# Kernel optimization log

Hardware: AMD Instinct MI355X
Metric: run time of the kernel (lower is better)

Reference implementation:

```python
import jax, jax.numpy as jnp
import numpy as np

B = 4096
N = 8192
LEVEL_SIZES = [8, 128, 2048, 6008]  # sums to N; 4-level taxonomy
EPS = 1e-07


def _build_hierarchy():
    """parent[c] = parent node index (-1 for roots); level_of[c] = depth."""
    rng = np.random.default_rng(0)
    parent = np.full(N, -1, np.int32)
    level_of = np.zeros(N, np.int32)
    off, prev_start, prev_size = 0, 0, 0
    for l, sz in enumerate(LEVEL_SIZES):
        level_of[off:off + sz] = l
        if l > 0:
            parent[off:off + sz] = rng.integers(prev_start, prev_start + prev_size, sz)
        prev_start, prev_size = off, sz
        off += sz
    return parent, level_of


def setup_inputs() -> dict:
    key = jax.random.key(0)
    k1, k2 = jax.random.split(key)
    pred = jax.random.normal(k1, (B, N), dtype=jnp.float32)  # logits
    target = (jax.random.uniform(k2, (B, N)) < 0.02).astype(jnp.float32)
    parent_np, level_np = _build_hierarchy()
    return {
        "pred": pred,
        "target": target,
        "parent": jnp.asarray(parent_np),
        "level_of": jnp.asarray(level_np),
        "mode": 0,  # 0 = EVAL (propagate conditional probs), 1 = TRAIN
    }


def reference(pred, target, parent, level_of, mode):
    p = jax.nn.sigmoid(pred)                      # [B, N]
    parent_clip = jnp.maximum(parent, 0)          # safe gather index for roots
    is_root = parent < 0                          # recursive_relation[-1]

    if mode != 1:  # not 'TRAIN': top-down conditional probability propagation
        pc = p
        for l in range(1, len(LEVEL_SIZES)):
            # pred_clone[:, children(n)] = pred[:, children] * pred_clone[:, n]
            pc = jnp.where(level_of == l, p * pc[:, parent_clip], pc)
        pred_clone = pc
    else:
        pred_clone = None

    # mask[b, c] = 1 if c is a root, or if target[b, parent[c]] == 1
    mask = jnp.where(is_root, jnp.float32(1.0), target[:, parent_clip])

    pcl = jnp.clip(p, EPS, 1.0 - EPS)
    loss = -(jnp.log(pcl) * target + (1.0 - target) * mask * jnp.log(1.0 - pcl))
    loss = loss.sum(axis=1).mean()
    return (loss, pred_clone)
```

## Files before the change

kernel.cpp:

```cpp
#include <hip/hip_runtime.h>


typedef float f4 __attribute__((ext_vector_type(4)));
typedef float f2 __attribute__((ext_vector_type(2)));
typedef int   i4 __attribute__((ext_vector_type(4)));

#define N_NODES 8192
#define L1S 8
#define L2S 136
#define L3S 2184
#define N4   2048
#define L3S4 546
#define WPB 4

__device__ __forceinline__ float frcp(float x) { return __builtin_amdgcn_rcpf(x); }

__device__ __forceinline__ void wave_sync() {
    __builtin_amdgcn_sched_barrier(0);
    asm volatile("s_waitcnt lgkmcnt(0)" ::: "memory");
    __builtin_amdgcn_wave_barrier();
    __builtin_amdgcn_sched_barrier(0);
}

__global__ __launch_bounds__(256, 4) void cs_main(
    const float* __restrict__ pred,
    const float* __restrict__ target,
    const int* __restrict__ parent,
    float* __restrict__ out,
    float* __restrict__ bsum,
    float inv_b, int nrows)
{
    __shared__ float pk_all[WPB * L3S];

    const int tid = threadIdx.x;
    const int lane = tid & 63;
    const int wid = tid >> 6;
    const int b = blockIdx.x * WPB + wid;
    if (b >= nrows) return;

    float* __restrict__ mypk = pk_all + wid * L3S;
    const float* __restrict__ prow = pred + (size_t)b * N_NODES;
    const float* __restrict__ trow = target + (size_t)b * N_NODES;
    float* __restrict__ orow = out + 1 + (size_t)b * N_NODES;
    const f4* __restrict__ Pp = (const f4*)prow;
    const f4* __restrict__ Tp = (const f4*)trow;
    const i4* __restrict__ Qp = (const i4*)parent;

    float lsum = 0.0f;

    {
        int g = lane;
        f4 x4 = Pp[g], t4 = Tp[g];
#pragma unroll
        for (int k = 0; k < 9; ++k) {
            const int gn = g + 64;
            f4 nx, nt;
            const bool hn = (gn < L3S4);
            if (hn) { nx = Pp[gn]; nt = Tp[gn]; }
            if (g < L3S4) {
                f4 pkv;
#pragma unroll
                for (int j = 0; j < 4; ++j) {
                    const float p = frcp(1.0f + __expf(-x4[j]));
                    pkv[j] = t4[j] > 0.5f ? -p : p;
                }
                *(f4*)(mypk + 4 * g) = pkv;
            }
            x4 = nx; t4 = nt; g = gn;
        }
    }

    int gc = L3S4 + lane;
    f4 xA = Pp[gc], tA = Tp[gc]; i4 qA = Qp[gc];
    const int g1 = gc + 64;
    f4 xB = Pp[g1], tB = Tp[g1]; i4 qB = Qp[g1];

    wave_sync();

    if (lane < L1S) {
        const float v = mypk[lane];
        const float p = fabsf(v);
        lsum += (v < 0.0f) ? -__logf(p) : -__logf(1.0f - p);
        orow[lane] = p;
    }

#pragma unroll
    for (int k = 0; k < 2; ++k) {
        const int c = L1S + lane + 64 * k;
        const int pa = parent[c];
        const float v = mypk[c];
        const float pv = mypk[pa];
        const float p = fabsf(v);
        const float cum = p * fabsf(pv);
        const float mask = (pv < 0.0f) ? 1.0f : 0.0f;
        lsum += (v < 0.0f) ? -__logf(p) : mask * (-__logf(1.0f - p));
        orow[c] = cum;
        mypk[c] = (v < 0.0f) ? -cum : cum;
    }
    wave_sync();

#pragma unroll 4
    for (int k = 0; k < 32; ++k) {
        const int c = L2S + lane + 64 * k;
        const int pa = parent[c];
        const float v = mypk[c];
        const float pv = mypk[pa];
        const float p = fabsf(v);
        const float cum = p * fabsf(pv);
        const float mask = (pv < 0.0f) ? 1.0f : 0.0f;
        lsum += (v < 0.0f) ? -__logf(p) : mask * (-__logf(1.0f - p));
        orow[c] = cum;
        mypk[c] = (v < 0.0f) ? -cum : cum;
    }
    wave_sync();

#pragma unroll 4
    for (int k = 0; k < 24; ++k) {
        const int gn = gc + 128 > N4 - 1 ? N4 - 1 : gc + 128;
        f4 nx = Pp[gn], nt = Tp[gn]; i4 nq = Qp[gn];
        if (gc < N4) {
            float rr[4];
#pragma unroll
            for (int j = 0; j < 4; ++j) {
                const float x = xA[j], t = tA[j];
                const float pv = mypk[qA[j]];
                const float mask = (pv < 0.0f) ? 1.0f : 0.0f;
                const float e = __expf(-x);
                const float s = __logf(1.0f + e);
                const float p = frcp(1.0f + e);
                lsum += t * s + (1.0f - t) * mask * (s + x);
                rr[j] = p * fabsf(pv);
            }
            float* slot = orow + 4 * gc;
            slot[0] = rr[0];
            *(f2*)(slot + 1) = f2{rr[1], rr[2]};
            slot[3] = rr[3];
        }
        xA = xB; tA = tB; qA = qB;
        xB = nx; tB = nt; qB = nq;
        gc += 64;
    }

#pragma unroll
    for (int off = 32; off > 0; off >>= 1) lsum += __shfl_down(lsum, off);
    if (lane == 0) {
        if (bsum) bsum[b] = lsum;
        else atomicAdd(out, lsum * inv_b);
    }
}

__global__ __launch_bounds__(256) void cs_finish(
    const float* __restrict__ bsum, float* __restrict__ out,
    int n, float inv_b)
{
    __shared__ float red[4];
    const int tid = threadIdx.x;
    float s = 0.0f;
    for (int i = tid; i < n; i += 256) s += bsum[i];
#pragma unroll
    for (int off = 32; off > 0; off >>= 1) s += __shfl_down(s, off);
    if ((tid & 63) == 0) red[tid >> 6] = s;
    __syncthreads();
    if (tid == 0) out[0] = ((red[0] + red[1]) + (red[2] + red[3])) * inv_b;
}

extern "C" void kernel_launch(void* const* d_in, const int* in_sizes, int n_in,
                              void* d_out, int out_size, void* d_ws, size_t ws_size,
                              hipStream_t stream) {
    const float* pred   = (const float*)d_in[0];
    const float* target = (const float*)d_in[1];
    const int*   parent = (const int*)d_in[2];

    float* out = (float*)d_out;
    const int batch = in_sizes[0] / N_NODES;
    const float inv_b = 1.0f / (float)batch;
    const int nblk = (batch + WPB - 1) / WPB;

    if (ws_size >= (size_t)batch * sizeof(float)) {
        float* bsum = (float*)d_ws;
        cs_main<<<nblk, 256, 0, stream>>>(pred, target, parent, out, bsum, inv_b, batch);
        cs_finish<<<1, 256, 0, stream>>>(bsum, out, batch, inv_b);
    } else {
        hipMemsetAsync(d_out, 0, sizeof(float), stream);
        cs_main<<<nblk, 256, 0, stream>>>(pred, target, parent, out, nullptr, inv_b, batch);
    }
}
```

Baseline: 99.47 us.

## Split leaf-level processing into a separate high-occupancy streaming kernel

The row kernel now handles only the top three levels. A new kernel, launched over batch times six tiles, processes the 6008 leaf nodes. It reads each parent's cumulative probability back from the output written by the first kernel, and reads the parent's target directly from global memory instead of from LDS. Leaf stores are realigned with a lane shuffle so each lane writes one aligned float4. The aim is more parallelism and occupancy on the bandwidth-bound leaf portion, at the cost of an extra launch, re-reading level-3 outputs, and more partial sums to reduce.

Measured after the change: 177.9 us. +78.8%, slower.

```diff
diff --git a/kernel.cpp b/kernel.cpp
--- a/kernel.cpp
+++ b/kernel.cpp
@@ -12,6 +12,7 @@
 #define N4   2048
 #define L3S4 546
 #define WPB 4
+#define TILES 6
 
 __device__ __forceinline__ float frcp(float x) { return __builtin_amdgcn_rcpf(x); }
 
@@ -22,12 +23,13 @@
     __builtin_amdgcn_sched_barrier(0);
 }
 
-__global__ __launch_bounds__(256, 4) void cs_main(
+__global__ __launch_bounds__(256, 4) void cs_small(
     const float* __restrict__ pred,
     const float* __restrict__ target,
     const int* __restrict__ parent,
     float* __restrict__ out,
     float* __restrict__ bsum,
+    float* __restrict__ outp,
     float inv_b, int nrows)
 {
     __shared__ float pk_all[WPB * L3S];
@@ -44,7 +46,6 @@
     float* __restrict__ orow = out + 1 + (size_t)b * N_NODES;
     const f4* __restrict__ Pp = (const f4*)prow;
     const f4* __restrict__ Tp = (const f4*)trow;
-    const i4* __restrict__ Qp = (const i4*)parent;
 
     float lsum = 0.0f;
 
@@ -55,8 +56,7 @@
         for (int k = 0; k < 9; ++k) {
             const int gn = g + 64;
             f4 nx, nt;
-            const bool hn = (gn < L3S4);
-            if (hn) { nx = Pp[gn]; nt = Tp[gn]; }
+            if (gn < L3S4) { nx = Pp[gn]; nt = Tp[gn]; }
             if (g < L3S4) {
                 f4 pkv;
 #pragma unroll
@@ -69,12 +69,6 @@
             x4 = nx; t4 = nt; g = gn;
         }
     }
-
-    int gc = L3S4 + lane;
-    f4 xA = Pp[gc], tA = Tp[gc]; i4 qA = Qp[gc];
-    const int g1 = gc + 64;
-    f4 xB = Pp[g1], tB = Tp[g1]; i4 qB = Qp[g1];
-
     wave_sync();
 
     if (lane < L1S) {
@@ -110,42 +104,73 @@
         const float mask = (pv < 0.0f) ? 1.0f : 0.0f;
         lsum += (v < 0.0f) ? -__logf(p) : mask * (-__logf(1.0f - p));
         orow[c] = cum;
-        mypk[c] = (v < 0.0f) ? -cum : cum;
-    }
-    wave_sync();
-
-#pragma unroll 4
-    for (int k = 0; k < 24; ++k) {
-        const int gn = gc + 128 > N4 - 1 ? N4 - 1 : gc + 128;
-        f4 nx = Pp[gn], nt = Tp[gn]; i4 nq = Qp[gn];
-        if (gc < N4) {
-            float rr[4];
-#pragma unroll
-            for (int j = 0; j < 4; ++j) {
-                const float x = xA[j], t = tA[j];
-                const float pv = mypk[qA[j]];
-                const float mask = (pv < 0.0f) ? 1.0f : 0.0f;
-                const float e = __expf(-x);
-                const float s = __logf(1.0f + e);
-                const float p = frcp(1.0f + e);
-                lsum += t * s + (1.0f - t) * mask * (s + x);
-                rr[j] = p * fabsf(pv);
-            }
-            float* slot = orow + 4 * gc;
-            slot[0] = rr[0];
-            *(f2*)(slot + 1) = f2{rr[1], rr[2]};
-            slot[3] = rr[3];
-        }
-        xA = xB; tA = tB; qA = qB;
-        xB = nx; tB = nt; qB = nq;
-        gc += 64;
     }
 
 #pragma unroll
     for (int off = 32; off > 0; off >>= 1) lsum += __shfl_down(lsum, off);
     if (lane == 0) {
         if (bsum) bsum[b] = lsum;
-        else atomicAdd(out, lsum * inv_b);
+        else atomicAdd(outp, lsum * inv_b);
+    }
+}
+
+__global__ __launch_bounds__(256, 8) void cs_stream(
+    const float* __restrict__ pred,
+    const float* __restrict__ target,
+    const int* __restrict__ parent,
+    float* __restrict__ out,
+    float* __restrict__ bsum2,
+    float inv_b)
+{
+    const int tid = threadIdx.x;
+    const int b = blockIdx.x / TILES;
+    const int t = blockIdx.x - b * TILES;
+    const int g = L3S4 + t * 256 + tid;
+    const int lane = tid & 63;
+
+    const float* __restrict__ prow = pred + (size_t)b * N_NODES;
+    const float* __restrict__ trow = target + (size_t)b * N_NODES;
+    float* __restrict__ obase = out + (size_t)b * N_NODES;
+
+    float lsum = 0.0f;
+    if (g < N4) {
+        const f4 x4 = ((const f4*)prow)[g];
+        const f4 t4 = ((const f4*)trow)[g];
+        const i4 q4 = ((const i4*)parent)[g];
+        float rr[4];
+#pragma unroll
+        for (int j = 0; j < 4; ++j) {
+            const float x = x4[j], t_ = t4[j];
+            const int pa = q4[j];
+            const float cum = obase[pa + 1];
+            const float mask = trow[pa];
+            const float e = __expf(-x);
+            const float s = __logf(1.0f + e);
+            const float p = frcp(1.0f + e);
+            lsum += t_ * s + (1.0f - t_) * mask * (s + x);
+            rr[j] = p * cum;
+        }
+        const float prev3 = __shfl_up(rr[3], 1);
+        float* slot = obase + 4 * g;
+        if (lane > 0) {
+            f4 v = {prev3, rr[0], rr[1], rr[2]};
+            *(f4*)slot = v;
+        } else {
+            slot[1] = rr[0];
+            *(f2*)(slot + 2) = f2{rr[1], rr[2]};
+        }
+        if (lane == 63 || g == N4 - 1) slot[4] = rr[3];
+    }
+
+    __shared__ float red[4];
+#pragma unroll
+    for (int off = 32; off > 0; off >>= 1) lsum += __shfl_down(lsum, off);
+    if ((tid & 63) == 0) red[tid >> 6] = lsum;
+    __syncthreads();
+    if (tid == 0) {
+        const float s = (red[0] + red[1]) + (red[2] + red[3]);
+        if (bsum2) bsum2[blockIdx.x] = s;
+        else atomicAdd(out, s * inv_b);
     }
 }
 
@@ -174,14 +199,22 @@
     float* out = (float*)d_out;
     const int batch = in_sizes[0] / N_NODES;
     const float inv_b = 1.0f / (float)batch;
-    const int nblk = (batch + WPB - 1) / WPB;
-
-    if (ws_size >= (size_t)batch * sizeof(float)) {
+    const int nblk1 = (batch + WPB - 1) / WPB;
+    const int nblk2 = batch * TILES;
+    const int npart = batch + nblk2;
+
+    if (ws_size >= (size_t)npart * sizeof(float)) {
         float* bsum = (float*)d_ws;
-        cs_main<<<nblk, 256, 0, stream>>>(pred, target, parent, out, bsum, inv_b, batch);
-        cs_finish<<<1, 256, 0, stream>>>(bsum, out, batch, inv_b);
+        cs_small<<<nblk1, 256, 0, stream>>>(pred, target, parent, out, bsum,
+                                            nullptr, inv_b, batch);
+        cs_stream<<<nblk2, 256, 0, stream>>>(pred, target, parent, out,
+                                             bsum + batch, inv_b);
+        cs_finish<<<1, 256, 0, stream>>>(bsum, out, npart, inv_b);
     } else {
         hipMemsetAsync(d_out, 0, sizeof(float), stream);
-        cs_main<<<nblk, 256, 0, stream>>>(pred, target, parent, out, nullptr, inv_b, batch);
-    }
-}
+        cs_small<<<nblk1, 256, 0, stream>>>(pred, target, parent, out, nullptr,
+                                            out, inv_b, batch);
+        cs_stream<<<nblk2, 256, 0, stream>>>(pred, target, parent, out,
+                                             nullptr, inv_b);
+    }
+}
```
